# Kernel tuning notes

Hardware: AMD Instinct MI355X
Metric: run time of the kernel (lower is better)

Reference implementation:

```python
import jax, jax.numpy as jnp
import numpy as np

D_MODEL = 512
N_HEADS = 8
D_K = D_MODEL // N_HEADS


def setup_inputs() -> dict:
    key = jax.random.key(0)
    ks = jax.random.split(key, 11)
    B, L, D = 2, 4096, D_MODEL
    s = 1.0 / np.sqrt(D)
    return {
        "q": jax.random.normal(ks[0], (B, L, D), jnp.float32),
        "k": jax.random.normal(ks[1], (B, L, D), jnp.float32),
        "v": jax.random.normal(ks[2], (B, L, D), jnp.float32),
        "Wq": jax.random.normal(ks[3], (D, D), jnp.float32) * s,
        "bq": jnp.zeros((D,), jnp.float32),
        "Wk": jax.random.normal(ks[4], (D, D), jnp.float32) * s,
        "bk": jnp.zeros((D,), jnp.float32),
        "Wv": jax.random.normal(ks[5], (D, D), jnp.float32) * s,
        "bv": jnp.zeros((D,), jnp.float32),
        "Wo": jax.random.normal(ks[6], (D, D), jnp.float32) * s,
        "bo": jnp.zeros((D,), jnp.float32),
    }


def reference(q, k, v, Wq, bq, Wk, bk, Wv, bv, Wo, bo):
    B, L, D = q.shape
    H, dk = N_HEADS, D_K
    # projections -> [B, H, L, dk]
    qh = (q @ Wq + bq).reshape(B, L, H, dk).transpose(0, 2, 1, 3)
    kh = (k @ Wk + bk).reshape(B, -1, H, dk).transpose(0, 2, 1, 3)
    vh = (v @ Wv + bv).reshape(B, -1, H, dk).transpose(0, 2, 1, 3)
    scores = jnp.einsum("bhqd,bhkd->bhqk", qh, kh) / jnp.sqrt(jnp.float32(dk))
    attn = jax.nn.softmax(scores, axis=-1)  # dropout: eval-mode identity
    ctx = jnp.einsum("bhqk,bhkd->bhqd", attn, vh)
    ctx = ctx.transpose(0, 2, 1, 3).reshape(B, L, D)
    return ctx @ Wo + bo
```

## Files before the change

### kernel.cpp

```cpp
#include <hip/hip_runtime.h>
#include <hip/hip_bf16.h>

#define NB 2
#define NL 4096
#define ND 512
#define NH 8
#define NDK 64
#define NM (NB * NL)
#define QSCALE 0.18033688011112042f

typedef short bf16x8_t __attribute__((ext_vector_type(8)));
typedef float f32x4_t __attribute__((ext_vector_type(4)));

static __device__ __forceinline__ unsigned short f2bs(float f) {
  union { float f; unsigned u; } c; c.f = f;
  unsigned r = c.u + 0x7fffu + ((c.u >> 16) & 1u);
  return (unsigned short)(r >> 16);
}
static __device__ __forceinline__ float bs2f(unsigned short s) {
  union { unsigned u; float f; } c; c.u = ((unsigned)s) << 16; return c.f;
}
static __device__ __forceinline__ unsigned pk_bf16(float a, float b) {
  union { __hip_bfloat162 h; unsigned u; } c;
  c.h = __float22bfloat162_rn(make_float2(a, b));
  return c.u;
}
static __device__ __forceinline__ unsigned cvt_pk_hw(float a, float b) {
  unsigned r;
  asm("v_cvt_pk_bf16_f32 %0, %1, %2" : "=v"(r) : "v"(a), "v"(b));
  return r;
}

struct WArgs {
  const float* W[4];
  unsigned short* Th[4];
  unsigned short* Tl[4];
};
__global__ __launch_bounds__(256)
void wsplit_kernel(WArgs a)
{
  const int z = blockIdx.z;
  const float* __restrict__ W = a.W[z];
  const int tid = threadIdx.x;
  const int n = blockIdx.x * 64 + (tid & 63);
  const int kb = blockIdx.y * 64 + (tid >> 6) * 16;
  unsigned short h[16], l[16];
#pragma unroll
  for (int u = 0; u < 16; ++u) {
    const float x = W[(size_t)(kb + u) * ND + n];
    h[u] = f2bs(x);
    l[u] = f2bs(x - bs2f(h[u]));
  }
  unsigned wh[8], wl[8];
#pragma unroll
  for (int p = 0; p < 8; ++p) {
    wh[p] = (unsigned)h[2 * p] | ((unsigned)h[2 * p + 1] << 16);
    wl[p] = (unsigned)l[2 * p] | ((unsigned)l[2 * p + 1] << 16);
  }
  unsigned short* th = a.Th[z] + (size_t)n * ND + kb;
  unsigned short* tl = a.Tl[z] + (size_t)n * ND + kb;
  *(uint4*)th = make_uint4(wh[0], wh[1], wh[2], wh[3]);
  *(uint4*)(th + 8) = make_uint4(wh[4], wh[5], wh[6], wh[7]);
  *(uint4*)tl = make_uint4(wl[0], wl[1], wl[2], wl[3]);
  *(uint4*)(tl + 8) = make_uint4(wl[4], wl[5], wl[6], wl[7]);
}

template <bool ASPLIT, int NJ, int OUTMODE, int WI, int WJ, bool AFP32>
__device__ __forceinline__ void gemm_core(
    const void* __restrict__ Ahi_, const unsigned short* __restrict__ Alo,
    const unsigned short* __restrict__ Bh, const unsigned short* __restrict__ Bl,
    const float* __restrict__ bias, unsigned short* __restrict__ outH,
    float* __restrict__ outF, int m0, int n0, float scale)
{
  static_assert(!(ASPLIT && AFP32), "unsupported combo");
  constexpr int WGC = NJ / WJ;
  static_assert((4 / WGC) * WI * 16 == 128, "wave grid must tile 128 rows");
  static_assert(OUTMODE == 1 || (WI == 4 && WJ == 4 && WGC == 2),
                "epilogues 0/2 assume 2x2 wave grid");

  __shared__ unsigned short AH[128][36];
  __shared__ unsigned short AL[ASPLIT ? 128 : 1][36];
  __shared__ unsigned short BHs[NJ * 16][36];
  __shared__ unsigned short BLs[NJ * 16][36];

  const int tid = threadIdx.x;
  const int lane = tid & 63, w = tid >> 6;
  const int m = lane & 15, quad = lane >> 4;
  const int wr = w / WGC, wc = w % WGC;
  const int r = tid >> 1, hf = (tid & 1) * 16;
  const int rb = (NJ == 8) ? (tid >> 1) : (tid >> 2);
  const int cb = (NJ == 8) ? ((tid & 1) * 16) : ((tid & 3) * 8);

  const unsigned short* aRow = nullptr;
  const float* aRowF = nullptr;
  if constexpr (AFP32)
    aRowF = (const float*)Ahi_ + (size_t)(m0 + r) * ND + hf;
  else
    aRow = (const unsigned short*)Ahi_ + (size_t)(m0 + r) * ND + hf;
  const unsigned short* alRow = ASPLIT ? (Alo + (size_t)(m0 + r) * ND + hf) : nullptr;
  const unsigned short* bhRow = Bh + (size_t)(n0 + rb) * ND + cb;
  const unsigned short* blRow = Bl + (size_t)(n0 + rb) * ND + cb;

  uint4 ra0, ra1;
  float4 fa0, fa1, fa2, fa3;
  if constexpr (AFP32) {
    fa0 = *(const float4*)(aRowF);
    fa1 = *(const float4*)(aRowF + 4);
    fa2 = *(const float4*)(aRowF + 8);
    fa3 = *(const float4*)(aRowF + 12);
  } else {
    ra0 = *(const uint4*)(aRow);
    ra1 = *(const uint4*)(aRow + 8);
  }
  uint4 rl0, rl1;
  if constexpr (ASPLIT) {
    rl0 = *(const uint4*)(alRow);
    rl1 = *(const uint4*)(alRow + 8);
  }
  uint4 rbh0 = *(const uint4*)(bhRow);
  uint4 rbl0 = *(const uint4*)(blRow);
  uint4 rbh1, rbl1;
  if constexpr (NJ == 8) {
    rbh1 = *(const uint4*)(bhRow + 8);
    rbl1 = *(const uint4*)(blRow + 8);
  }

  f32x4_t acc[WI][WJ];
#pragma unroll
  for (int i = 0; i < WI; ++i)
#pragma unroll
    for (int j = 0; j < WJ; ++j) acc[i][j] = (f32x4_t){0.f, 0.f, 0.f, 0.f};

  for (int k0 = 0; k0 < ND; k0 += 32) {
    __syncthreads();
    if constexpr (AFP32) {
      uint4 ua0, ua1;
      ua0.x = pk_bf16(fa0.x, fa0.y);
      ua0.y = pk_bf16(fa0.z, fa0.w);
      ua0.z = pk_bf16(fa1.x, fa1.y);
      ua0.w = pk_bf16(fa1.z, fa1.w);
      ua1.x = pk_bf16(fa2.x, fa2.y);
      ua1.y = pk_bf16(fa2.z, fa2.w);
      ua1.z = pk_bf16(fa3.x, fa3.y);
      ua1.w = pk_bf16(fa3.z, fa3.w);
      *(uint4*)&AH[r][hf] = ua0;
      *(uint4*)&AH[r][hf + 8] = ua1;
    } else {
      *(uint4*)&AH[r][hf] = ra0;
      *(uint4*)&AH[r][hf + 8] = ra1;
    }
    if constexpr (ASPLIT) {
      *(uint4*)&AL[r][hf] = rl0;
      *(uint4*)&AL[r][hf + 8] = rl1;
    }
    *(uint4*)&BHs[rb][cb] = rbh0;
    *(uint4*)&BLs[rb][cb] = rbl0;
    if constexpr (NJ == 8) {
      *(uint4*)&BHs[rb][cb + 8] = rbh1;
      *(uint4*)&BLs[rb][cb + 8] = rbl1;
    }
    if (k0 + 32 < ND) {
      const int kn = k0 + 32;
      if constexpr (AFP32) {
        fa0 = *(const float4*)(aRowF + kn);
        fa1 = *(const float4*)(aRowF + kn + 4);
        fa2 = *(const float4*)(aRowF + kn + 8);
        fa3 = *(const float4*)(aRowF + kn + 12);
      } else {
        ra0 = *(const uint4*)(aRow + kn);
        ra1 = *(const uint4*)(aRow + kn + 8);
      }
      if constexpr (ASPLIT) {
        rl0 = *(const uint4*)(alRow + kn);
        rl1 = *(const uint4*)(alRow + kn + 8);
      }
      rbh0 = *(const uint4*)(bhRow + kn);
      rbl0 = *(const uint4*)(blRow + kn);
      if constexpr (NJ == 8) {
        rbh1 = *(const uint4*)(bhRow + kn + 8);
        rbl1 = *(const uint4*)(blRow + kn + 8);
      }
    }
    __syncthreads();

    bf16x8_t ah[WI], al[ASPLIT ? WI : 1];
#pragma unroll
    for (int i = 0; i < WI; ++i) {
      ah[i] = *(const bf16x8_t*)&AH[wr * (WI * 16) + 16 * i + m][quad * 8];
      if constexpr (ASPLIT)
        al[i] = *(const bf16x8_t*)&AL[wr * (WI * 16) + 16 * i + m][quad * 8];
    }
#pragma unroll
    for (int j = 0; j < WJ; ++j) {
      const bf16x8_t bhj = *(const bf16x8_t*)&BHs[16 * (wc * WJ + j) + m][quad * 8];
      const bf16x8_t blj = *(const bf16x8_t*)&BLs[16 * (wc * WJ + j) + m][quad * 8];
#pragma unroll
      for (int i = 0; i < WI; ++i) {
        acc[i][j] = __builtin_amdgcn_mfma_f32_16x16x32_bf16(ah[i], bhj, acc[i][j], 0, 0, 0);
        acc[i][j] = __builtin_amdgcn_mfma_f32_16x16x32_bf16(ah[i], blj, acc[i][j], 0, 0, 0);
        if constexpr (ASPLIT)
          acc[i][j] = __builtin_amdgcn_mfma_f32_16x16x32_bf16(al[i], bhj, acc[i][j], 0, 0, 0);
      }
    }
  }

  if constexpr (OUTMODE == 1) {
#pragma unroll
    for (int i = 0; i < WI; ++i)
#pragma unroll
      for (int rr = 0; rr < 4; ++rr) {
        const int mg = m0 + wr * (WI * 16) + 16 * i + quad * 4 + rr;
#pragma unroll
        for (int j = 0; j < WJ; ++j) {
          const int n = n0 + 16 * (wc * WJ + j) + m;
          outF[(size_t)mg * ND + n] = (acc[i][j][rr] + bias[n]) * scale;
        }
      }
  } else if constexpr (OUTMODE == 0) {
    unsigned short* T = &BHs[0][0];
    const int bb = m0 >> 12;
#pragma unroll
    for (int p = 0; p < 4; ++p) {
      __syncthreads();
      if (wr == (p >> 1)) {
#pragma unroll
        for (int i2 = 0; i2 < 2; ++i2) {
          const int i = (p & 1) * 2 + i2;
#pragma unroll
          for (int j = 0; j < WJ; ++j) {
            const int n = wc * 64 + 16 * j + m;
            const float bv = bias[n0 + n];
#pragma unroll
            for (int rr = 0; rr < 4; ++rr)
              T[(16 * i2 + quad * 4 + rr) * 136 + n] =
                  f2bs((acc[i][j][rr] + bv) * scale);
          }
        }
      }
      __syncthreads();
      const int lr = tid >> 3;
      const int seg = tid & 7;
      const uint4 t0 = *(const uint4*)&T[lr * 136 + seg * 16];
      const uint4 t1 = *(const uint4*)&T[lr * 136 + seg * 16 + 8];
      const int ng = n0 + seg * 16;
      const int h = ng >> 6, d = ng & (NDK - 1);
      const int l = (m0 + p * 32 + lr) & (NL - 1);
      unsigned short* dp = outH + (((size_t)(bb * NH + h)) * NL + l) * NDK + d;
      *(uint4*)dp = t0;
      *(uint4*)(dp + 8) = t1;
    }
  } else {
    unsigned short* T = &BHs[0][0];
    const int bb = m0 >> 12;
    const int lbase = m0 & (NL - 1);
#pragma unroll
    for (int p = 0; p < 4; ++p) {
      __syncthreads();
      if (wr == (p >> 1)) {
#pragma unroll
        for (int i2 = 0; i2 < 2; ++i2) {
          const int i = (p & 1) * 2 + i2;
#pragma unroll
          for (int j = 0; j < WJ; ++j) {
            const int n = wc * 64 + 16 * j + m;
            const float bv = bias[n0 + n];
            const unsigned w0 = pk_bf16((acc[i][j][0] + bv) * scale,
                                        (acc[i][j][1] + bv) * scale);
            const unsigned w1 = pk_bf16((acc[i][j][2] + bv) * scale,
                                        (acc[i][j][3] + bv) * scale);
            *(uint2*)&T[n * 34 + 16 * i2 + quad * 4] = make_uint2(w0, w1);
          }
        }
      }
      __syncthreads();
      const int n = tid >> 1;
      const int l0 = (tid & 1) * 16;
      const uint4 t0 = *(const uint4*)&T[n * 34 + l0];
      const uint4 t1 = *(const uint4*)&T[n * 34 + l0 + 8];
      const int ng = n0 + n;
      const int h = ng >> 6, d = ng & (NDK - 1);
      unsigned short* dp =
          outH + (((size_t)(bb * NH + h)) * NDK + d) * NL + lbase + 32 * p + l0;
      *(uint4*)dp = t0;
      *(uint4*)(dp + 8) = t1;
    }
  }
}

struct ProjArgs {
  const float* A[3];
  const unsigned short* Bh[3];
  const unsigned short* Bl[3];
  const float* bias[3];
  unsigned short* out[3];
  float scale[3];
};
__global__ __launch_bounds__(256, 3)
void gemm_proj_kernel(ProjArgs a)
{
  const int z = blockIdx.z;
  if (z < 2)
    gemm_core<false, 8, 0, 4, 4, true>(a.A[z], nullptr, a.Bh[z], a.Bl[z],
                                       a.bias[z], a.out[z], nullptr,
                                       blockIdx.x * 128, blockIdx.y * 128, a.scale[z]);
  else
    gemm_core<false, 8, 2, 4, 4, true>(a.A[2], nullptr, a.Bh[2], a.Bl[2],
                                       a.bias[2], a.out[2], nullptr,
                                       blockIdx.x * 128, blockIdx.y * 128, a.scale[2]);
}
__global__ __launch_bounds__(256, 3)
void gemm_out_kernel(const unsigned short* __restrict__ Ahi,
                     const unsigned short* __restrict__ Alo,
                     const unsigned short* __restrict__ Bh,
                     const unsigned short* __restrict__ Bl,
                     const float* __restrict__ bias, float* __restrict__ out)
{
  gemm_core<true, 4, 1, 2, 4, false>(Ahi, Alo, Bh, Bl, bias, nullptr, out,
                                     blockIdx.x * 128, blockIdx.y * 64, 1.0f);
}

__global__ __launch_bounds__(256, 2)
void attn_kernel(const unsigned short* __restrict__ qh, const unsigned short* __restrict__ kh,
                 const unsigned short* __restrict__ vt_g, float* __restrict__ op,
                 float* __restrict__ lp)
{
  __shared__ unsigned short Ks[2][64 * 64];
  __shared__ unsigned short Vt[2][64 * 64];

  const int tid = threadIdx.x;
  const int w = tid >> 6;
  const int lane = tid & 63;
  const int m = lane & 15;
  const int quad = lane >> 4;
  const int sw = m & 7;

  const int bid = blockIdx.x;
  const int half = bid & 1;
  const int qt = (bid >> 1) & 15;
  const int bh = bid >> 5;
  const int kt0 = half * 32, kt1 = kt0 + 32;
  const unsigned short* qb = qh + (size_t)bh * NL * NDK;
  const unsigned short* kb = kh + (size_t)bh * NL * NDK;
  const unsigned short* vb = vt_g + (size_t)bh * NDK * NL;

  bf16x8_t aq[4][2];
#pragma unroll
  for (int mt = 0; mt < 4; ++mt) {
    const unsigned short* qsrc =
        qb + (size_t)(qt * 256 + w * 64 + mt * 16 + m) * NDK + quad * 8;
    aq[mt][0] = *(const bf16x8_t*)(qsrc);
    aq[mt][1] = *(const bf16x8_t*)(qsrc + 32);
  }

  const short ob = (short)0x3F80;
  const bf16x8_t ones = {ob, ob, ob, ob, ob, ob, ob, ob};

  f32x4_t o[4][4];
#pragma unroll
  for (int mt = 0; mt < 4; ++mt)
#pragma unroll
    for (int nt = 0; nt < 4; ++nt) o[mt][nt] = (f32x4_t){0.f, 0.f, 0.f, 0.f};
  f32x4_t ol[4];
#pragma unroll
  for (int mt = 0; mt < 4; ++mt) ol[mt] = (f32x4_t){0.f, 0.f, 0.f, 0.f};

  const int kr = tid >> 2;
  const int kcb = tid & 3;
  const int kc = kcb * 16;
  const int r7 = kr & 7;
  const int st0 = kr * 64 + ((2 * kcb) ^ r7) * 8;
  const int st1 = kr * 64 + ((2 * kcb + 1) ^ r7) * 8;

  const int rowb = m * 64;
  const int ck0 = rowb + ((quad ^ sw) * 8);
  const int ck1 = rowb + (((quad + 4) ^ sw) * 8);
  const int vq = quad >> 1, vo = (quad & 1) * 4;
  const int va0[2] = { rowb + vo + (((0 + vq) ^ sw) * 8),
                       rowb + vo + (((4 + vq) ^ sw) * 8) };
  const int va1[2] = { rowb + vo + (((2 + vq) ^ sw) * 8),
                       rowb + vo + (((6 + vq) ^ sw) * 8) };

  const unsigned short* kptr = kb + (size_t)(kt0 * 64 + kr) * NDK + kc;
  const unsigned short* vptr = vb + (size_t)kr * NL + kt0 * 64 + kc;
  uint4 pk0 = *(const uint4*)kptr;
  uint4 pk1 = *(const uint4*)(kptr + 8);
  uint4 pv0 = *(const uint4*)vptr;
  uint4 pv1 = *(const uint4*)(vptr + 8);
  *(uint4*)&Ks[0][st0] = pk0;
  *(uint4*)&Ks[0][st1] = pk1;
  *(uint4*)&Vt[0][st0] = pv0;
  *(uint4*)&Vt[0][st1] = pv1;
  kptr += 64 * NDK;
  vptr += 64;
  pk0 = *(const uint4*)kptr;
  pk1 = *(const uint4*)(kptr + 8);
  pv0 = *(const uint4*)vptr;
  pv1 = *(const uint4*)(vptr + 8);
  __syncthreads();

#define ATTN_STEP(B, W, KT)                                                   \
  {                                                                           \
            \
    f32x4_t s[4][4];                                            \
    _Pragma("unroll")                                                         \
    for (int nt = 0; nt < 4; ++nt) {                                          \
      const bf16x8_t kf0 = *(const bf16x8_t*)&Ks[B][nt * 1024 + ck0];         \
      const bf16x8_t kf1 = *(const bf16x8_t*)&Ks[B][nt * 1024 + ck1];         \
      _Pragma("unroll")                                                       \
      for (int mt = 0; mt < 4; ++mt) {                                        \
        f32x4_t s_ = (f32x4_t){0.f, 0.f, 0.f, 0.f};                           \
        s_ = __builtin_amdgcn_mfma_f32_16x16x32_bf16(kf0, aq[mt][0], s_, 0, 0, 0); \
        s_ = __builtin_amdgcn_mfma_f32_16x16x32_bf16(kf1, aq[mt][1], s_, 0, 0, 0); \
        s[nt][mt] = s_;                                                       \
      }                                                                       \
    }                                                                         \
    __builtin_amdgcn_sched_barrier(0);   \
    _Pragma("unroll")                                                         \
    for (int c = 0; c < 2; ++c) {                                             \
      union U { bf16x8_t v; unsigned d[4]; };                                 \
      U pa[4];                                                                \
      _Pragma("unroll")                                                       \
      for (int mt = 0; mt < 4; ++mt) {                                        \
        pa[mt].d[0] = cvt_pk_hw(__builtin_amdgcn_exp2f(s[2 * c][mt][0]),      \
                                __builtin_amdgcn_exp2f(s[2 * c][mt][1]));     \
        pa[mt].d[1] = cvt_pk_hw(__builtin_amdgcn_exp2f(s[2 * c][mt][2]),      \
                                __builtin_amdgcn_exp2f(s[2 * c][mt][3]));     \
        pa[mt].d[2] = cvt_pk_hw(__builtin_amdgcn_exp2f(s[2 * c + 1][mt][0]),  \
                                __builtin_amdgcn_exp2f(s[2 * c + 1][mt][1])); \
        pa[mt].d[3] = cvt_pk_hw(__builtin_amdgcn_exp2f(s[2 * c + 1][mt][2]),  \
                                __builtin_amdgcn_exp2f(s[2 * c + 1][mt][3])); \
      }                                                                       \
      __builtin_amdgcn_s_setprio(1);                                          \
      _Pragma("unroll")                                                       \
      for (int nt = 0; nt < 4; ++nt) {                                        \
        union { bf16x8_t v; uint2 h[2]; } vf;                                 \
        vf.h[0] = *(const uint2*)&Vt[B][nt * 1024 + va0[c]];                  \
        vf.h[1] = *(const uint2*)&Vt[B][nt * 1024 + va1[c]];                  \
        _Pragma("unroll")                                                     \
        for (int mt = 0; mt < 4; ++mt)                                        \
          o[mt][nt] = __builtin_amdgcn_mfma_f32_16x16x32_bf16(pa[mt].v, vf.v, \
                                                              o[mt][nt], 0, 0, 0); \
      }                                                                       \
      _Pragma("unroll")                                                       \
      for (int mt = 0; mt < 4; ++mt)                                          \
        ol[mt] = __builtin_amdgcn_mfma_f32_16x16x32_bf16(pa[mt].v, ones,      \
                                                         ol[mt], 0, 0, 0);    \
      __builtin_amdgcn_s_setprio(0);                                          \
    }                                                                         \
    if ((KT) + 1 < kt1) {                                                     \
      *(uint4*)&Ks[W][st0] = pk0;                                             \
      *(uint4*)&Ks[W][st1] = pk1;                                             \
      *(uint4*)&Vt[W][st0] = pv0;                                             \
      *(uint4*)&Vt[W][st1] = pv1;                                             \
      if ((KT) + 2 < kt1) {                                                   \
        kptr += 64 * NDK;                                                     \
        vptr += 64;                                                           \
        pk0 = *(const uint4*)kptr;                                            \
        pk1 = *(const uint4*)(kptr + 8);                                      \
        pv0 = *(const uint4*)vptr;                                            \
        pv1 = *(const uint4*)(vptr + 8);                                      \
      }                                                                       \
      __syncthreads();                                                        \
    }                                                                         \
  }

  for (int kt = kt0; kt < kt1; kt += 2) {
    ATTN_STEP(0, 1, kt);
    ATTN_STEP(1, 0, kt + 1);
  }
#undef ATTN_STEP

  const size_t pbase = (size_t)(half * 16 + bh) * NL;
#pragma unroll
  for (int mt = 0; mt < 4; ++mt) {
    const int q0 = qt * 256 + w * 64 + mt * 16 + quad * 4;
    if (m == 0)
      *(float4*)&lp[pbase + q0] =
          make_float4(ol[mt][0], ol[mt][1], ol[mt][2], ol[mt][3]);
#pragma unroll
    for (int r = 0; r < 4; ++r) {
      float* dst = op + (pbase + q0 + r) * NDK;
#pragma unroll
      for (int nt = 0; nt < 4; ++nt) dst[16 * nt + m] = o[mt][nt][r];
    }
  }
}

__global__ __launch_bounds__(256)
void merge_kernel(const float* __restrict__ op, const float* __restrict__ lp,
                  unsigned short* __restrict__ ctxh, unsigned short* __restrict__ ctxl)
{
  const size_t t = (size_t)blockIdx.x * 256 + threadIdx.x;
  const int d0 = (int)(t & 7) * 8;
  const size_t row = t >> 3;
  const float l0 = lp[row];
  const float l1 = lp[row + (size_t)16 * NL];
  const float inv = 1.0f / (l0 + l1);
  const float* a = op + row * NDK + d0;
  const float* c = a + (size_t)16 * NL * NDK;
  const float4 a0 = *(const float4*)a, a1 = *(const float4*)(a + 4);
  const float4 c0 = *(const float4*)c, c1 = *(const float4*)(c + 4);
  const float x[8] = {(a0.x + c0.x) * inv, (a0.y + c0.y) * inv,
                      (a0.z + c0.z) * inv, (a0.w + c0.w) * inv,
                      (a1.x + c1.x) * inv, (a1.y + c1.y) * inv,
                      (a1.z + c1.z) * inv, (a1.w + c1.w) * inv};
  unsigned short hs[8], ls[8];
#pragma unroll
  for (int u = 0; u < 8; ++u) {
    hs[u] = f2bs(x[u]);
    ls[u] = f2bs(x[u] - bs2f(hs[u]));
  }
  const int bh = (int)(row >> 12), l = (int)(row & (NL - 1));
  const int b = bh >> 3, h = bh & 7;
  const size_t dst = ((size_t)(b * NL + l)) * ND + h * 64 + d0;
  uint4 uh, ul;
  uh.x = (unsigned)hs[0] | ((unsigned)hs[1] << 16);
  uh.y = (unsigned)hs[2] | ((unsigned)hs[3] << 16);
  uh.z = (unsigned)hs[4] | ((unsigned)hs[5] << 16);
  uh.w = (unsigned)hs[6] | ((unsigned)hs[7] << 16);
  ul.x = (unsigned)ls[0] | ((unsigned)ls[1] << 16);
  ul.y = (unsigned)ls[2] | ((unsigned)ls[3] << 16);
  ul.z = (unsigned)ls[4] | ((unsigned)ls[5] << 16);
  ul.w = (unsigned)ls[6] | ((unsigned)ls[7] << 16);
  *(uint4*)(ctxh + dst) = uh;
  *(uint4*)(ctxl + dst) = ul;
}

extern "C" void kernel_launch(void* const* d_in, const int* in_sizes, int n_in,
                              void* d_out, int out_size, void* d_ws, size_t ws_size,
                              hipStream_t stream)
{
  const float* q  = (const float*)d_in[0];
  const float* k  = (const float*)d_in[1];
  const float* v  = (const float*)d_in[2];
  const float* Wq = (const float*)d_in[3];
  const float* bq = (const float*)d_in[4];
  const float* Wk = (const float*)d_in[5];
  const float* bk = (const float*)d_in[6];
  const float* Wv = (const float*)d_in[7];
  const float* bv = (const float*)d_in[8];
  const float* Wo = (const float*)d_in[9];
  const float* bo = (const float*)d_in[10];

  const size_t PLANE = (size_t)NM * ND;
  unsigned short* wt = (unsigned short*)d_ws;
  unsigned short* qhp = wt + 8 * (size_t)ND * ND;
  unsigned short* khp = qhp + PLANE;
  unsigned short* vtp = khp + PLANE;
  float* op = (float*)(vtp + PLANE);
  float* lp = op + 2 * (size_t)16 * NL * NDK;
  unsigned short* ctxh = qhp;
  unsigned short* ctxl = khp;

  unsigned short* wth[4], *wtl[4];
  for (int i = 0; i < 4; ++i) {
    wth[i] = wt + (size_t)(2 * i) * ND * ND;
    wtl[i] = wt + (size_t)(2 * i + 1) * ND * ND;
  }

  WArgs wa;
  wa.W[0] = Wq; wa.W[1] = Wk; wa.W[2] = Wv; wa.W[3] = Wo;
  for (int i = 0; i < 4; ++i) { wa.Th[i] = wth[i]; wa.Tl[i] = wtl[i]; }
  wsplit_kernel<<<dim3(8, 8, 4), 256, 0, stream>>>(wa);

  ProjArgs pa;
  pa.A[0] = q; pa.A[1] = k; pa.A[2] = v;
  pa.Bh[0] = wth[0]; pa.Bl[0] = wtl[0];
  pa.Bh[1] = wth[1]; pa.Bl[1] = wtl[1];
  pa.Bh[2] = wth[2]; pa.Bl[2] = wtl[2];
  pa.bias[0] = bq; pa.bias[1] = bk; pa.bias[2] = bv;
  pa.out[0] = qhp; pa.out[1] = khp; pa.out[2] = vtp;
  pa.scale[0] = QSCALE; pa.scale[1] = 1.0f; pa.scale[2] = 1.0f;
  gemm_proj_kernel<<<dim3(NM / 128, ND / 128, 3), 256, 0, stream>>>(pa);

  attn_kernel<<<dim3(NB * NH * (NL / 256) * 2), 256, 0, stream>>>(qhp, khp, vtp, op, lp);

  merge_kernel<<<dim3((16 * NL * NDK) / (256 * 8)), 256, 0, stream>>>(op, lp, ctxh, ctxl);

  gemm_out_kernel<<<dim3(NM / 128, ND / 64), 256, 0, stream>>>(
      ctxh, ctxl, wth[3], wtl[3], bo, (float*)d_out);
}
```

Before: 245.3 us.

## Fuse split-KV merge and hi/lo split into output projection GEMM

Removes the separate merge kernel. The output GEMM now reads the two fp32 attention partials and their row sums directly, normalises them, and splits the result into bf16 hi/lo tiles while staging A into shared memory. This drops one launch and the round-trip of the intermediate bf16 context planes through global memory. In exchange, each column block re-reads the larger fp32 partials. Those loads are issued at the top of each k-step instead of being prefetched a step ahead, so more load latency may be exposed.

```diff
diff --git a/kernel.cpp b/kernel.cpp
--- a/kernel.cpp
+++ b/kernel.cpp
@@ -29,6 +29,12 @@
   unsigned r;
   asm("v_cvt_pk_bf16_f32 %0, %1, %2" : "=v"(r) : "v"(a), "v"(b));
   return r;
+}
+static __device__ __forceinline__ void split_pk(float a, float b,
+                                                unsigned& hw, unsigned& lw) {
+  const unsigned short ha = f2bs(a), hb = f2bs(b);
+  hw = (unsigned)ha | ((unsigned)hb << 16);
+  lw = (unsigned)f2bs(a - bs2f(ha)) | ((unsigned)f2bs(b - bs2f(hb)) << 16);
 }
 
 struct WArgs {
@@ -65,14 +71,16 @@
   *(uint4*)(tl + 8) = make_uint4(wl[4], wl[5], wl[6], wl[7]);
 }
 
-template <bool ASPLIT, int NJ, int OUTMODE, int WI, int WJ, bool AFP32>
+template <bool ASPLIT, int NJ, int OUTMODE, int WI, int WJ, bool AFP32, bool AMERGE>
 __device__ __forceinline__ void gemm_core(
     const void* __restrict__ Ahi_, const unsigned short* __restrict__ Alo,
     const unsigned short* __restrict__ Bh, const unsigned short* __restrict__ Bl,
     const float* __restrict__ bias, unsigned short* __restrict__ outH,
-    float* __restrict__ outF, int m0, int n0, float scale)
+    float* __restrict__ outF, int m0, int n0, float scale,
+    const float* __restrict__ opA, const float* __restrict__ lpA)
 {
   static_assert(!(ASPLIT && AFP32), "unsupported combo");
+  static_assert(!(AFP32 && AMERGE), "unsupported combo");
   constexpr int WGC = NJ / WJ;
   static_assert((4 / WGC) * WI * 16 == 128, "wave grid must tile 128 rows");
   static_assert(OUTMODE == 1 || (WI == 4 && WJ == 4 && WGC == 2),
@@ -95,11 +103,18 @@
   const float* aRowF = nullptr;
   if constexpr (AFP32)
     aRowF = (const float*)Ahi_ + (size_t)(m0 + r) * ND + hf;
-  else
+  else if constexpr (!AMERGE)
     aRow = (const unsigned short*)Ahi_ + (size_t)(m0 + r) * ND + hf;
-  const unsigned short* alRow = ASPLIT ? (Alo + (size_t)(m0 + r) * ND + hf) : nullptr;
+  const unsigned short* alRow =
+      (ASPLIT && !AMERGE) ? (Alo + (size_t)(m0 + r) * ND + hf) : nullptr;
   const unsigned short* bhRow = Bh + (size_t)(n0 + rb) * ND + cb;
   const unsigned short* blRow = Bl + (size_t)(n0 + rb) * ND + cb;
+
+  int abb = 0, all = 0;
+  if constexpr (AMERGE) {
+    abb = (m0 + r) >> 12;
+    all = (m0 + r) & (NL - 1);
+  }
 
   uint4 ra0, ra1;
   float4 fa0, fa1, fa2, fa3;
@@ -108,12 +123,12 @@
     fa1 = *(const float4*)(aRowF + 4);
     fa2 = *(const float4*)(aRowF + 8);
     fa3 = *(const float4*)(aRowF + 12);
-  } else {
+  } else if constexpr (!AMERGE) {
     ra0 = *(const uint4*)(aRow);
     ra1 = *(const uint4*)(aRow + 8);
   }
   uint4 rl0, rl1;
-  if constexpr (ASPLIT) {
+  if constexpr (ASPLIT && !AMERGE) {
     rl0 = *(const uint4*)(alRow);
     rl1 = *(const uint4*)(alRow + 8);
   }
@@ -132,8 +147,43 @@
     for (int j = 0; j < WJ; ++j) acc[i][j] = (f32x4_t){0.f, 0.f, 0.f, 0.f};
 
   for (int k0 = 0; k0 < ND; k0 += 32) {
+    float4 a00, a01, a02, a03, a10, a11, a12, a13;
+    float li0, li1;
+    if constexpr (AMERGE) {
+      const int kk = k0 + hf;
+      const int head = kk >> 6;
+      const int d0 = kk & (NDK - 1);
+      const size_t prow = (size_t)(abb * 8 + head) * NL + all;
+      const float* p0 = opA + prow * NDK + d0;
+      const float* p1 = p0 + (size_t)16 * NL * NDK;
+      a00 = *(const float4*)p0;
+      a01 = *(const float4*)(p0 + 4);
+      a02 = *(const float4*)(p0 + 8);
+      a03 = *(const float4*)(p0 + 12);
+      a10 = *(const float4*)p1;
+      a11 = *(const float4*)(p1 + 4);
+      a12 = *(const float4*)(p1 + 8);
+      a13 = *(const float4*)(p1 + 12);
+      li0 = lpA[prow];
+      li1 = lpA[prow + (size_t)16 * NL];
+    }
     __syncthreads();
-    if constexpr (AFP32) {
+    if constexpr (AMERGE) {
+      const float inv = 1.0f / (li0 + li1);
+      uint4 uh0, ul0, uh1, ul1;
+      split_pk((a00.x + a10.x) * inv, (a00.y + a10.y) * inv, uh0.x, ul0.x);
+      split_pk((a00.z + a10.z) * inv, (a00.w + a10.w) * inv, uh0.y, ul0.y);
+      split_pk((a01.x + a11.x) * inv, (a01.y + a11.y) * inv, uh0.z, ul0.z);
+      split_pk((a01.z + a11.z) * inv, (a01.w + a11.w) * inv, uh0.w, ul0.w);
+      split_pk((a02.x + a12.x) * inv, (a02.y + a12.y) * inv, uh1.x, ul1.x);
+      split_pk((a02.z + a12.z) * inv, (a02.w + a12.w) * inv, uh1.y, ul1.y);
+      split_pk((a03.x + a13.x) * inv, (a03.y + a13.y) * inv, uh1.z, ul1.z);
+      split_pk((a03.z + a13.z) * inv, (a03.w + a13.w) * inv, uh1.w, ul1.w);
+      *(uint4*)&AH[r][hf] = uh0;
+      *(uint4*)&AH[r][hf + 8] = uh1;
+      *(uint4*)&AL[r][hf] = ul0;
+      *(uint4*)&AL[r][hf + 8] = ul1;
+    } else if constexpr (AFP32) {
       uint4 ua0, ua1;
       ua0.x = pk_bf16(fa0.x, fa0.y);
       ua0.y = pk_bf16(fa0.z, fa0.w);
@@ -149,7 +199,7 @@
       *(uint4*)&AH[r][hf] = ra0;
       *(uint4*)&AH[r][hf + 8] = ra1;
     }
-    if constexpr (ASPLIT) {
+    if constexpr (ASPLIT && !AMERGE) {
       *(uint4*)&AL[r][hf] = rl0;
       *(uint4*)&AL[r][hf + 8] = rl1;
     }
@@ -166,11 +216,11 @@
         fa1 = *(const float4*)(aRowF + kn + 4);
         fa2 = *(const float4*)(aRowF + kn + 8);
         fa3 = *(const float4*)(aRowF + kn + 12);
-      } else {
+      } else if constexpr (!AMERGE) {
         ra0 = *(const uint4*)(aRow + kn);
         ra1 = *(const uint4*)(aRow + kn + 8);
       }
-      if constexpr (ASPLIT) {
+      if constexpr (ASPLIT && !AMERGE) {
         rl0 = *(const uint4*)(alRow + kn);
         rl1 = *(const uint4*)(alRow + kn + 8);
       }
@@ -300,23 +350,23 @@
 {
   const int z = blockIdx.z;
   if (z < 2)
-    gemm_core<false, 8, 0, 4, 4, true>(a.A[z], nullptr, a.Bh[z], a.Bl[z],
-                                       a.bias[z], a.out[z], nullptr,
-                                       blockIdx.x * 128, blockIdx.y * 128, a.scale[z]);
+    gemm_core<false, 8, 0, 4, 4, true, false>(
+        a.A[z], nullptr, a.Bh[z], a.Bl[z], a.bias[z], a.out[z], nullptr,
+        blockIdx.x * 128, blockIdx.y * 128, a.scale[z], nullptr, nullptr);
   else
-    gemm_core<false, 8, 2, 4, 4, true>(a.A[2], nullptr, a.Bh[2], a.Bl[2],
-                                       a.bias[2], a.out[2], nullptr,
-                                       blockIdx.x * 128, blockIdx.y * 128, a.scale[2]);
+    gemm_core<false, 8, 2, 4, 4, true, false>(
+        a.A[2], nullptr, a.Bh[2], a.Bl[2], a.bias[2], a.out[2], nullptr,
+        blockIdx.x * 128, blockIdx.y * 128, a.scale[2], nullptr, nullptr);
 }
 __global__ __launch_bounds__(256, 3)
-void gemm_out_kernel(const unsigned short* __restrict__ Ahi,
-                     const unsigned short* __restrict__ Alo,
+void gemm_out_kernel(const float* __restrict__ opA, const float* __restrict__ lpA,
                      const unsigned short* __restrict__ Bh,
                      const unsigned short* __restrict__ Bl,
                      const float* __restrict__ bias, float* __restrict__ out)
 {
-  gemm_core<true, 4, 1, 2, 4, false>(Ahi, Alo, Bh, Bl, bias, nullptr, out,
-                                     blockIdx.x * 128, blockIdx.y * 64, 1.0f);
+  gemm_core<true, 4, 1, 2, 4, false, true>(
+      nullptr, nullptr, Bh, Bl, bias, nullptr, out,
+      blockIdx.x * 128, blockIdx.y * 64, 1.0f, opA, lpA);
 }
 
 __global__ __launch_bounds__(256, 2)
@@ -486,46 +536,6 @@
   }
 }
 
-__global__ __launch_bounds__(256)
-void merge_kernel(const float* __restrict__ op, const float* __restrict__ lp,
-                  unsigned short* __restrict__ ctxh, unsigned short* __restrict__ ctxl)
-{
-  const size_t t = (size_t)blockIdx.x * 256 + threadIdx.x;
-  const int d0 = (int)(t & 7) * 8;
-  const size_t row = t >> 3;
-  const float l0 = lp[row];
-  const float l1 = lp[row + (size_t)16 * NL];
-  const float inv = 1.0f / (l0 + l1);
-  const float* a = op + row * NDK + d0;
-  const float* c = a + (size_t)16 * NL * NDK;
-  const float4 a0 = *(const float4*)a, a1 = *(const float4*)(a + 4);
-  const float4 c0 = *(const float4*)c, c1 = *(const float4*)(c + 4);
-  const float x[8] = {(a0.x + c0.x) * inv, (a0.y + c0.y) * inv,
-                      (a0.z + c0.z) * inv, (a0.w + c0.w) * inv,
-                      (a1.x + c1.x) * inv, (a1.y + c1.y) * inv,
-                      (a1.z + c1.z) * inv, (a1.w + c1.w) * inv};
-  unsigned short hs[8], ls[8];
-#pragma unroll
-  for (int u = 0; u < 8; ++u) {
-    hs[u] = f2bs(x[u]);
-    ls[u] = f2bs(x[u] - bs2f(hs[u]));
-  }
-  const int bh = (int)(row >> 12), l = (int)(row & (NL - 1));
-  const int b = bh >> 3, h = bh & 7;
-  const size_t dst = ((size_t)(b * NL + l)) * ND + h * 64 + d0;
-  uint4 uh, ul;
-  uh.x = (unsigned)hs[0] | ((unsigned)hs[1] << 16);
-  uh.y = (unsigned)hs[2] | ((unsigned)hs[3] << 16);
-  uh.z = (unsigned)hs[4] | ((unsigned)hs[5] << 16);
-  uh.w = (unsigned)hs[6] | ((unsigned)hs[7] << 16);
-  ul.x = (unsigned)ls[0] | ((unsigned)ls[1] << 16);
-  ul.y = (unsigned)ls[2] | ((unsigned)ls[3] << 16);
-  ul.z = (unsigned)ls[4] | ((unsigned)ls[5] << 16);
-  ul.w = (unsigned)ls[6] | ((unsigned)ls[7] << 16);
-  *(uint4*)(ctxh + dst) = uh;
-  *(uint4*)(ctxl + dst) = ul;
-}
-
 extern "C" void kernel_launch(void* const* d_in, const int* in_sizes, int n_in,
                               void* d_out, int out_size, void* d_ws, size_t ws_size,
                               hipStream_t stream)
@@ -549,8 +559,6 @@
   unsigned short* vtp = khp + PLANE;
   float* op = (float*)(vtp + PLANE);
   float* lp = op + 2 * (size_t)16 * NL * NDK;
-  unsigned short* ctxh = qhp;
-  unsigned short* ctxl = khp;
 
   unsigned short* wth[4], *wtl[4];
   for (int i = 0; i < 4; ++i) {
@@ -575,8 +583,6 @@
 
   attn_kernel<<<dim3(NB * NH * (NL / 256) * 2), 256, 0, stream>>>(qhp, khp, vtp, op, lp);
 
-  merge_kernel<<<dim3((16 * NL * NDK) / (256 * 8)), 256, 0, stream>>>(op, lp, ctxh, ctxl);
-
   gemm_out_kernel<<<dim3(NM / 128, ND / 64), 256, 0, stream>>>(
-      ctxh, ctxl, wth[3], wtl[3], bo, (float*)d_out);
-}
+      op, lp, wth[3], wtl[3], bo, (float*)d_out);
+}
```

Result: no change. 243.5 us (-0.7%).
